# Optimization experiments

Hardware: AMD Instinct MI355X
Metric: run time of the kernel (lower is better)

The kernel has to match this reference:

```python
import jax, jax.numpy as jnp
import numpy as np

H = 8     # n_head_qk == n_head_v
DF = 32   # d_fix_qk == d_fix_v

def setup_inputs() -> dict:
    key = jax.random.key(0)
    k0, k1, k2, k3, k4 = jax.random.split(key, 5)
    x = jax.random.normal(k0, (2, 2048, 128), jnp.float32)
    attn_bias = jax.random.normal(k1, (1, H, 2048, 2048), jnp.float32) * 0.1
    Wqkv = jax.random.normal(k2, (3 * H * DF, 128), jnp.float32) * 0.02   # nn.Linear(d_model, 3*h*df)
    Wtalk = jax.random.normal(k3, (H, H), jnp.float32) * 0.1              # 1x1 Conv2d over head channels
    Wproj = jax.random.normal(k4, (128, H * DF), jnp.float32) * 0.02      # nn.Linear(h*df_v, d_model)
    return {"x": x, "attn_bias": attn_bias, "Wqkv": Wqkv, "Wtalk": Wtalk, "Wproj": Wproj}

def reference(x, attn_bias, Wqkv, Wtalk, Wproj):
    B, P, D = x.shape
    # qkv: [B,P,3*H*DF] -> [3,B,H,P,DF]
    qkv = (x @ Wqkv.T).reshape(B, P, 3, H, DF).transpose(2, 0, 3, 1, 4)
    scale = jnp.sqrt(jnp.asarray(DF, x.dtype))
    q, k, v = qkv[0] / scale, qkv[1], qkv[2]
    attn = jnp.einsum('bhpd,bhqd->bhpq', q, k)          # [B,H,P,P]
    attn = jnp.einsum('gh,bhpq->bgpq', Wtalk, attn)     # talking-heads 1x1 conv
    attn = jax.nn.softmax(attn + attn_bias, axis=-1)
    out = jnp.einsum('bhpq,bhqd->bhpd', attn, v)        # [B,H,P,DF]
    out = out.transpose(0, 2, 1, 3).reshape(B, P, H * DF)
    return out @ Wproj.T                                 # [B,P,D]
```

## Files before the change

### kernel.cpp

```cpp
#include <hip/hip_runtime.h>


typedef __attribute__((ext_vector_type(8))) short short8v;
typedef __attribute__((ext_vector_type(4))) float f32x4;

static __device__ __forceinline__ unsigned short f2bf(float f) {
  union { float f; unsigned u; } v; v.f = f;
  return (unsigned short)((v.u + 0x7FFFu + ((v.u >> 16) & 1u)) >> 16);
}

#define RAW_BARRIER() do { \
  asm volatile("s_waitcnt lgkmcnt(0)" ::: "memory"); \
  __builtin_amdgcn_sched_barrier(0); \
  __builtin_amdgcn_s_barrier(); \
  __builtin_amdgcn_sched_barrier(0); \
} while (0)

__global__ __launch_bounds__(256) void qkv_kernel(
    const float* __restrict__ x, const float* __restrict__ Wqkv,
    unsigned short* __restrict__ q_ws, unsigned short* __restrict__ k_ws,
    unsigned short* __restrict__ v_t) {
  __shared__ float xl[8][128];
  const int tid = threadIdx.x;
  const int rowbase = blockIdx.x * 8;
  {
    int r = tid >> 5, k4 = (tid & 31) * 4;
    *(float4*)&xl[r][k4] = *(const float4*)&x[(size_t)(rowbase + r) * 128 + k4];
  }
  __syncthreads();
  float acc[8][3];
#pragma unroll
  for (int r = 0; r < 8; ++r) { acc[r][0] = 0.f; acc[r][1] = 0.f; acc[r][2] = 0.f; }
  const float* w0p = &Wqkv[(size_t)tid * 128];
  const float* w1p = &Wqkv[(size_t)(tid + 256) * 128];
  const float* w2p = &Wqkv[(size_t)(tid + 512) * 128];
  for (int k4 = 0; k4 < 128; k4 += 4) {
    float4 w0 = *(const float4*)&w0p[k4];
    float4 w1 = *(const float4*)&w1p[k4];
    float4 w2 = *(const float4*)&w2p[k4];
#pragma unroll
    for (int r = 0; r < 8; ++r) {
      float4 xv = *(const float4*)&xl[r][k4];
      acc[r][0] += xv.x * w0.x + xv.y * w0.y + xv.z * w0.z + xv.w * w0.w;
      acc[r][1] += xv.x * w1.x + xv.y * w1.y + xv.z * w1.z + xv.w * w1.w;
      acc[r][2] += xv.x * w2.x + xv.y * w2.y + xv.z * w2.z + xv.w * w2.w;
    }
  }
  const int h = tid >> 5, d = tid & 31;
#pragma unroll
  for (int r = 0; r < 8; ++r) {
    int row = rowbase + r, b = row >> 11, pp = row & 2047;
    size_t base = ((size_t)(b * 8 + h) * 2048 + pp) * 32 + d;
    q_ws[base] = f2bf(acc[r][0] * 0.17677669529663687f);
    k_ws[base] = f2bf(acc[r][1]);
    v_t[((size_t)(b * 8 + h) * 32 + d) * 2048 + pp] = f2bf(acc[r][2]);
  }
}

template <int SPLIT>
__global__ __launch_bounds__(256, 2) void attn_kernel(
    const unsigned short* __restrict__ q_ws, const unsigned short* __restrict__ k_ws,
    const unsigned short* __restrict__ v_t, const float* __restrict__ bias,
    const float* __restrict__ Wtalk, float* __restrict__ pm, float* __restrict__ pl,
    float* __restrict__ pO) {
  constexpr int NB = 64 / SPLIT;
  __shared__ __align__(16) float Sb[8 * 1088];
  __shared__ __align__(16) unsigned short Pb[8192];

  const int qt_blk = blockIdx.x, split = blockIdx.y, b = blockIdx.z;
  const int q0 = qt_blk * 32, kv0 = split * (2048 / SPLIT);
  const int tid = threadIdx.x, w = tid >> 6, l = tid & 63, lg = l >> 4, ln = l & 15;
  const int p_mix = tid >> 3, qs = tid & 7, prow = q0 + p_mix;

  float wt[64];
#pragma unroll
  for (int i = 0; i < 64; ++i) wt[i] = Wtalk[i];

  short8v qf[2][2];
#pragma unroll
  for (int hh = 0; hh < 2; ++hh)
#pragma unroll
    for (int pt = 0; pt < 2; ++pt) {
      int h = 2 * w + hh;
      size_t a = ((size_t)((b * 8 + h) * 2048) + q0 + pt * 16 + ln) * 32 + lg * 8;
      qf[hh][pt] = *(const short8v*)&q_ws[a];
    }

  f32x4 Of[2][2][2];
#pragma unroll
  for (int hh = 0; hh < 2; ++hh)
#pragma unroll
    for (int pt = 0; pt < 2; ++pt)
#pragma unroll
      for (int dt = 0; dt < 2; ++dt) Of[hh][pt][dt] = (f32x4){0.f, 0.f, 0.f, 0.f};

  float mreg[8], lreg[8];
#pragma unroll
  for (int g = 0; g < 8; ++g) { mreg[g] = -1e30f; lreg[g] = 0.f; }

  const unsigned short *kB[2][2], *vB[2][2];
#pragma unroll
  for (int hh = 0; hh < 2; ++hh)
#pragma unroll
    for (int sc = 0; sc < 2; ++sc) {
      kB[hh][sc] = k_ws + ((size_t)(b * 8 + 2 * w + hh) * 2048 + kv0 + sc * 16 + ln) * 32 + lg * 8;
      vB[hh][sc] = v_t + ((size_t)(b * 8 + 2 * w + hh) * 32 + sc * 16 + ln) * 2048 + kv0 + lg * 8;
    }
  const float* bB = bias + (size_t)prow * 2048 + kv0 + qs * 4;

  short8v kf[2][2], vf[2][2];
  float4 bf[8];
#pragma unroll
  for (int hh = 0; hh < 2; ++hh)
#pragma unroll
    for (int sc = 0; sc < 2; ++sc) {
      kf[hh][sc] = *(const short8v*)kB[hh][sc];
      vf[hh][sc] = *(const short8v*)vB[hh][sc];
    }
#pragma unroll
  for (int g = 0; g < 8; ++g) bf[g] = *(const float4*)(bB + (size_t)g * 4194304);

#pragma unroll 2
  for (int s = 0; s < NB; ++s) {
    const int sn = (s + 1 < NB) ? s + 1 : s;

#pragma unroll
    for (int hh = 0; hh < 2; ++hh) {
      const int h_ = 2 * w + hh;
#pragma unroll
      for (int qt = 0; qt < 2; ++qt) {
#pragma unroll
        for (int pt = 0; pt < 2; ++pt) {
          f32x4 s4 = __builtin_amdgcn_mfma_f32_16x16x32_bf16(
              qf[hh][pt], kf[hh][qt], (f32x4){0.f, 0.f, 0.f, 0.f}, 0, 0, 0);
#pragma unroll
          for (int r = 0; r < 4; ++r)
            Sb[h_ * 1088 + (pt * 16 + lg * 4 + r) * 32 + qt * 16 + ln] = s4[r];
        }
      }
    }
    RAW_BARRIER();

    short8v kf_n[2][2];
#pragma unroll
    for (int hh = 0; hh < 2; ++hh)
#pragma unroll
      for (int sc = 0; sc < 2; ++sc)
        kf_n[hh][sc] = *(const short8v*)(kB[hh][sc] + (size_t)sn * 1024);

    {
      float4 sv[8];
#pragma unroll
      for (int h = 0; h < 8; ++h)
        sv[h] = *(const float4*)&Sb[h * 1088 + p_mix * 32 + qs * 4];
#pragma unroll
      for (int g = 0; g < 8; ++g) {
        float4 t4 = bf[g];
#pragma unroll
        for (int h = 0; h < 8; ++h) {
          const float wgh = wt[g * 8 + h];
          t4.x += wgh * sv[h].x; t4.y += wgh * sv[h].y;
          t4.z += wgh * sv[h].z; t4.w += wgh * sv[h].w;
        }
        float mx = fmaxf(fmaxf(t4.x, t4.y), fmaxf(t4.z, t4.w));
        mx = fmaxf(mx, __shfl_xor(mx, 1));
        mx = fmaxf(mx, __shfl_xor(mx, 2));
        mx = fmaxf(mx, __shfl_xor(mx, 4));
        const float mnew = fmaxf(mreg[g], mx);
        const float a_ = __expf(mreg[g] - mnew);
        mreg[g] = mnew;
        float ex = __expf(t4.x - mnew), ey = __expf(t4.y - mnew);
        float ez = __expf(t4.z - mnew), ew = __expf(t4.w - mnew);
        float ls = ex + ey + ez + ew;
        ls += __shfl_xor(ls, 1); ls += __shfl_xor(ls, 2); ls += __shfl_xor(ls, 4);
        lreg[g] = lreg[g] * a_ + ls;
        if (qs == 0) Sb[g * 1088 + 1024 + p_mix] = a_;
        unsigned u0 = (unsigned)f2bf(ex) | ((unsigned)f2bf(ey) << 16);
        unsigned u1 = (unsigned)f2bf(ez) | ((unsigned)f2bf(ew) << 16);
        uint2 pk; pk.x = u0; pk.y = u1;
        *(uint2*)&Pb[(size_t)((g * 2 + (p_mix >> 4)) * 64 + (qs >> 1) * 16 + (p_mix & 15)) * 8 + (qs & 1) * 4] = pk;
      }
    }

    float4 bf_n[8];
#pragma unroll
    for (int g = 0; g < 8; ++g)
      bf_n[g] = *(const float4*)(bB + (size_t)g * 4194304 + sn * 32);

    RAW_BARRIER();

#pragma unroll
    for (int hh = 0; hh < 2; ++hh) {
      const int h_ = 2 * w + hh;
#pragma unroll
      for (int pt = 0; pt < 2; ++pt) {
        float4 av = *(const float4*)&Sb[h_ * 1088 + 1024 + pt * 16 + lg * 4];
        short8v pa = *(const short8v*)&Pb[(size_t)((h_ * 2 + pt) * 64 + l) * 8];
#pragma unroll
        for (int dt = 0; dt < 2; ++dt) {
          f32x4 o = Of[hh][pt][dt];
          o[0] *= av.x; o[1] *= av.y; o[2] *= av.z; o[3] *= av.w;
          Of[hh][pt][dt] = __builtin_amdgcn_mfma_f32_16x16x32_bf16(pa, vf[hh][dt], o, 0, 0, 0);
        }
      }
    }

    short8v vf_n[2][2];
#pragma unroll
    for (int hh = 0; hh < 2; ++hh)
#pragma unroll
      for (int sc = 0; sc < 2; ++sc)
        vf_n[hh][sc] = *(const short8v*)(vB[hh][sc] + sn * 32);

#pragma unroll
    for (int hh = 0; hh < 2; ++hh)
#pragma unroll
      for (int sc = 0; sc < 2; ++sc) { kf[hh][sc] = kf_n[hh][sc]; vf[hh][sc] = vf_n[hh][sc]; }
#pragma unroll
    for (int g = 0; g < 8; ++g) bf[g] = bf_n[g];
  }

  const size_t ob = (size_t)((split * 2 + b) * 8);
#pragma unroll
  for (int hh = 0; hh < 2; ++hh)
#pragma unroll
    for (int pt = 0; pt < 2; ++pt)
#pragma unroll
      for (int dt = 0; dt < 2; ++dt)
#pragma unroll
        for (int r = 0; r < 4; ++r) {
          int h = 2 * w + hh;
          size_t idx = ((ob + h) * 2048 + q0 + pt * 16 + lg * 4 + r) * 32 + dt * 16 + ln;
          pO[idx] = Of[hh][pt][dt][r];
        }
  if (qs == 0) {
#pragma unroll
    for (int g = 0; g < 8; ++g) {
      size_t idx = (ob + g) * 2048 + prow;
      pm[idx] = mreg[g];
      pl[idx] = lreg[g];
    }
  }
}

template <int SPLIT>
__global__ __launch_bounds__(256) void comb_kernel(
    const float* __restrict__ pm, const float* __restrict__ pl,
    const float* __restrict__ pO, const float* __restrict__ Wproj,
    float* __restrict__ out) {
  __shared__ float ol[8][256];
  const int tid = threadIdx.x;
  const int rowbase = blockIdx.x * 8;
  {
    const int g = tid >> 5, d = tid & 31;
    for (int r = 0; r < 8; ++r) {
      int row = rowbase + r, b = row >> 11, p = row & 2047;
      size_t b0 = ((size_t)(b * 8 + g) * 2048 + p);
      float ms[SPLIT];
      float mx = -1e30f;
#pragma unroll
      for (int s = 0; s < SPLIT; ++s) {
        ms[s] = pm[b0 + (size_t)s * 32768];
        mx = fmaxf(mx, ms[s]);
      }
      float den = 0.f, acc = 0.f;
#pragma unroll
      for (int s = 0; s < SPLIT; ++s) {
        float ww = __expf(ms[s] - mx);
        den += ww * pl[b0 + (size_t)s * 32768];
        acc += ww * pO[(b0 + (size_t)s * 32768) * 32 + d];
      }
      ol[r][tid] = acc / den;
    }
  }
  __syncthreads();
  const int j = tid & 127, rh = tid >> 7;
  float acc[8];
#pragma unroll
  for (int r = 0; r < 8; ++r) acc[r] = 0.f;
  for (int c4 = 0; c4 < 128; c4 += 4) {
    float4 wv = *(const float4*)&Wproj[(size_t)j * 256 + rh * 128 + c4];
#pragma unroll
    for (int r = 0; r < 8; ++r) {
      float4 ov = *(const float4*)&ol[r][rh * 128 + c4];
      acc[r] += ov.x * wv.x + ov.y * wv.y + ov.z * wv.z + ov.w * wv.w;
    }
  }
  __syncthreads();
  float* red = &ol[0][0];
#pragma unroll
  for (int r = 0; r < 8; ++r) red[(r * 128 + j) * 2 + rh] = acc[r];
  __syncthreads();
#pragma unroll
  for (int rr = 0; rr < 4; ++rr) {
    int r = (tid >> 7) * 4 + rr;
    int row = rowbase + r;
    out[(size_t)row * 128 + (tid & 127)] =
        red[(r * 128 + (tid & 127)) * 2] + red[(r * 128 + (tid & 127)) * 2 + 1];
  }
}

extern "C" void kernel_launch(void* const* d_in, const int* in_sizes, int n_in,
                              void* d_out, int out_size, void* d_ws, size_t ws_size,
                              hipStream_t stream) {
  const float* x     = (const float*)d_in[0];
  const float* bias  = (const float*)d_in[1];
  const float* Wqkv  = (const float*)d_in[2];
  const float* Wtalk = (const float*)d_in[3];
  const float* Wproj = (const float*)d_in[4];
  float* out = (float*)d_out;
  char* ws = (char*)d_ws;
  unsigned short* q_ws = (unsigned short*)(ws);
  unsigned short* k_ws = (unsigned short*)(ws + (2u << 20));
  unsigned short* v_t  = (unsigned short*)(ws + (4u << 20));

  const size_t base = 6291456;
  const size_t per_split = 4456448;
  int SPLIT = (ws_size >= base + 8 * per_split) ? 8
            : (ws_size >= base + 4 * per_split) ? 4 : 2;
  float* pm = (float*)(ws + base);
  float* pl = (float*)(ws + base + (size_t)SPLIT * 131072);
  float* pO = (float*)(ws + base + (size_t)SPLIT * 262144);

  qkv_kernel<<<512, 256, 0, stream>>>(x, Wqkv, q_ws, k_ws, v_t);
  if (SPLIT == 8) {
    attn_kernel<8><<<dim3(64, 8, 2), 256, 0, stream>>>(q_ws, k_ws, v_t, bias, Wtalk, pm, pl, pO);
    comb_kernel<8><<<512, 256, 0, stream>>>(pm, pl, pO, Wproj, out);
  } else if (SPLIT == 4) {
    attn_kernel<4><<<dim3(64, 4, 2), 256, 0, stream>>>(q_ws, k_ws, v_t, bias, Wtalk, pm, pl, pO);
    comb_kernel<4><<<512, 256, 0, stream>>>(pm, pl, pO, Wproj, out);
  } else {
    attn_kernel<2><<<dim3(64, 2, 2), 256, 0, stream>>>(q_ws, k_ws, v_t, bias, Wtalk, pm, pl, pO);
    comb_kernel<2><<<512, 256, 0, stream>>>(pm, pl, pO, Wproj, out);
  }
}
```

Baseline: 316.3 us.

## Store scores as bf16, lazy softmax rescale, raise occupancy, remap blocks, vectorize V store

The score staging buffer in shared memory now holds bf16 with a padded stride instead of fp32, and the rescale factors get their own small array. This shrinks LDS use, and launch bounds rise to three blocks per CU. The online softmax skips the max reduction and rescale unless some lane's local max exceeds the running max by more than 8, and the per-row sum reduction is deferred to after the loop. Blocks are remapped over a 2D grid that interleaves batches, and the V-transpose store in the QKV kernel is packed into one 16-byte write. The changes trade score precision (bf16 before the talking-heads mix) and slightly looser exponent bounds for less LDS, fewer shuffles and fewer exps.

```diff
diff --git a/kernel.cpp b/kernel.cpp
--- a/kernel.cpp
+++ b/kernel.cpp
@@ -3,10 +3,14 @@
 
 typedef __attribute__((ext_vector_type(8))) short short8v;
 typedef __attribute__((ext_vector_type(4))) float f32x4;
+typedef __attribute__((ext_vector_type(4))) unsigned short ushort4v;
 
 static __device__ __forceinline__ unsigned short f2bf(float f) {
   union { float f; unsigned u; } v; v.f = f;
   return (unsigned short)((v.u + 0x7FFFu + ((v.u >> 16) & 1u)) >> 16);
+}
+static __device__ __forceinline__ float bf2f(unsigned short s) {
+  return __uint_as_float(((unsigned)s) << 16);
 }
 
 #define RAW_BARRIER() do { \
@@ -47,27 +51,33 @@
     }
   }
   const int h = tid >> 5, d = tid & 31;
+  const int b0 = rowbase >> 11, pp0 = rowbase & 2047;
+  short8v vv;
 #pragma unroll
   for (int r = 0; r < 8; ++r) {
-    int row = rowbase + r, b = row >> 11, pp = row & 2047;
-    size_t base = ((size_t)(b * 8 + h) * 2048 + pp) * 32 + d;
+    size_t base = ((size_t)(b0 * 8 + h) * 2048 + pp0 + r) * 32 + d;
     q_ws[base] = f2bf(acc[r][0] * 0.17677669529663687f);
     k_ws[base] = f2bf(acc[r][1]);
-    v_t[((size_t)(b * 8 + h) * 32 + d) * 2048 + pp] = f2bf(acc[r][2]);
-  }
+    vv[r] = (short)f2bf(acc[r][2]);
+  }
+  *(short8v*)&v_t[((size_t)(b0 * 8 + h) * 32 + d) * 2048 + pp0] = vv;
 }
 
 template <int SPLIT>
-__global__ __launch_bounds__(256, 2) void attn_kernel(
+__global__ __launch_bounds__(256, 3) void attn_kernel(
     const unsigned short* __restrict__ q_ws, const unsigned short* __restrict__ k_ws,
     const unsigned short* __restrict__ v_t, const float* __restrict__ bias,
     const float* __restrict__ Wtalk, float* __restrict__ pm, float* __restrict__ pl,
     float* __restrict__ pO) {
   constexpr int NB = 64 / SPLIT;
-  __shared__ __align__(16) float Sb[8 * 1088];
+  __shared__ __align__(16) unsigned short Sb16[8 * 1152];
+  __shared__ __align__(16) float Al[256];
   __shared__ __align__(16) unsigned short Pb[8192];
 
-  const int qt_blk = blockIdx.x, split = blockIdx.y, b = blockIdx.z;
+  const int bx = blockIdx.x;
+  const int qt_blk = ((bx >> 4) << 3) | (bx & 7);
+  const int b = (bx >> 3) & 1;
+  const int split = blockIdx.y;
   const int q0 = qt_blk * 32, kv0 = split * (2048 / SPLIT);
   const int tid = threadIdx.x, w = tid >> 6, l = tid & 63, lg = l >> 4, ln = l & 15;
   const int p_mix = tid >> 3, qs = tid & 7, prow = q0 + p_mix;
@@ -135,7 +145,7 @@
               qf[hh][pt], kf[hh][qt], (f32x4){0.f, 0.f, 0.f, 0.f}, 0, 0, 0);
 #pragma unroll
           for (int r = 0; r < 4; ++r)
-            Sb[h_ * 1088 + (pt * 16 + lg * 4 + r) * 32 + qt * 16 + ln] = s4[r];
+            Sb16[h_ * 1152 + (pt * 16 + lg * 4 + r) * 36 + qt * 16 + ln] = f2bf(s4[r]);
         }
       }
     }
@@ -151,8 +161,11 @@
     {
       float4 sv[8];
 #pragma unroll
-      for (int h = 0; h < 8; ++h)
-        sv[h] = *(const float4*)&Sb[h * 1088 + p_mix * 32 + qs * 4];
+      for (int h = 0; h < 8; ++h) {
+        ushort4v raw = *(const ushort4v*)&Sb16[h * 1152 + p_mix * 36 + qs * 4];
+        sv[h].x = bf2f(raw.x); sv[h].y = bf2f(raw.y);
+        sv[h].z = bf2f(raw.z); sv[h].w = bf2f(raw.w);
+      }
 #pragma unroll
       for (int g = 0; g < 8; ++g) {
         float4 t4 = bf[g];
@@ -162,19 +175,22 @@
           t4.x += wgh * sv[h].x; t4.y += wgh * sv[h].y;
           t4.z += wgh * sv[h].z; t4.w += wgh * sv[h].w;
         }
-        float mx = fmaxf(fmaxf(t4.x, t4.y), fmaxf(t4.z, t4.w));
-        mx = fmaxf(mx, __shfl_xor(mx, 1));
-        mx = fmaxf(mx, __shfl_xor(mx, 2));
-        mx = fmaxf(mx, __shfl_xor(mx, 4));
-        const float mnew = fmaxf(mreg[g], mx);
-        const float a_ = __expf(mreg[g] - mnew);
-        mreg[g] = mnew;
-        float ex = __expf(t4.x - mnew), ey = __expf(t4.y - mnew);
-        float ez = __expf(t4.z - mnew), ew = __expf(t4.w - mnew);
-        float ls = ex + ey + ez + ew;
-        ls += __shfl_xor(ls, 1); ls += __shfl_xor(ls, 2); ls += __shfl_xor(ls, 4);
-        lreg[g] = lreg[g] * a_ + ls;
-        if (qs == 0) Sb[g * 1088 + 1024 + p_mix] = a_;
+        float lm = fmaxf(fmaxf(t4.x, t4.y), fmaxf(t4.z, t4.w));
+        float a_ = 1.0f;
+        if (!__all(lm <= mreg[g] + 8.0f)) {
+          float rm = lm;
+          rm = fmaxf(rm, __shfl_xor(rm, 1));
+          rm = fmaxf(rm, __shfl_xor(rm, 2));
+          rm = fmaxf(rm, __shfl_xor(rm, 4));
+          float mnew = fmaxf(mreg[g], rm);
+          a_ = __expf(mreg[g] - mnew);
+          mreg[g] = mnew;
+          lreg[g] *= a_;
+        }
+        float ex = __expf(t4.x - mreg[g]), ey = __expf(t4.y - mreg[g]);
+        float ez = __expf(t4.z - mreg[g]), ew = __expf(t4.w - mreg[g]);
+        lreg[g] += (ex + ey) + (ez + ew);
+        if (qs == 0) Al[g * 32 + p_mix] = a_;
         unsigned u0 = (unsigned)f2bf(ex) | ((unsigned)f2bf(ey) << 16);
         unsigned u1 = (unsigned)f2bf(ez) | ((unsigned)f2bf(ew) << 16);
         uint2 pk; pk.x = u0; pk.y = u1;
@@ -194,7 +210,7 @@
       const int h_ = 2 * w + hh;
 #pragma unroll
       for (int pt = 0; pt < 2; ++pt) {
-        float4 av = *(const float4*)&Sb[h_ * 1088 + 1024 + pt * 16 + lg * 4];
+        float4 av = *(const float4*)&Al[h_ * 32 + pt * 16 + lg * 4];
         short8v pa = *(const short8v*)&Pb[(size_t)((h_ * 2 + pt) * 64 + l) * 8];
 #pragma unroll
         for (int dt = 0; dt < 2; ++dt) {
@@ -218,6 +234,13 @@
       for (int sc = 0; sc < 2; ++sc) { kf[hh][sc] = kf_n[hh][sc]; vf[hh][sc] = vf_n[hh][sc]; }
 #pragma unroll
     for (int g = 0; g < 8; ++g) bf[g] = bf_n[g];
+  }
+
+#pragma unroll
+  for (int g = 0; g < 8; ++g) {
+    float ls = lreg[g];
+    ls += __shfl_xor(ls, 1); ls += __shfl_xor(ls, 2); ls += __shfl_xor(ls, 4);
+    lreg[g] = ls;
   }
 
   const size_t ob = (size_t)((split * 2 + b) * 8);
@@ -294,8 +317,8 @@
 #pragma unroll
   for (int rr = 0; rr < 4; ++rr) {
     int r = (tid >> 7) * 4 + rr;
-    int row = rowbase + r;
-    out[(size_t)row * 128 + (tid & 127)] =
+    int rrow = rowbase + r;
+    out[(size_t)rrow * 128 + (tid & 127)] =
         red[(r * 128 + (tid & 127)) * 2] + red[(r * 128 + (tid & 127)) * 2 + 1];
   }
 }
@@ -324,13 +347,13 @@
 
   qkv_kernel<<<512, 256, 0, stream>>>(x, Wqkv, q_ws, k_ws, v_t);
   if (SPLIT == 8) {
-    attn_kernel<8><<<dim3(64, 8, 2), 256, 0, stream>>>(q_ws, k_ws, v_t, bias, Wtalk, pm, pl, pO);
+    attn_kernel<8><<<dim3(128, 8), 256, 0, stream>>>(q_ws, k_ws, v_t, bias, Wtalk, pm, pl, pO);
     comb_kernel<8><<<512, 256, 0, stream>>>(pm, pl, pO, Wproj, out);
   } else if (SPLIT == 4) {
-    attn_kernel<4><<<dim3(64, 4, 2), 256, 0, stream>>>(q_ws, k_ws, v_t, bias, Wtalk, pm, pl, pO);
+    attn_kernel<4><<<dim3(128, 4), 256, 0, stream>>>(q_ws, k_ws, v_t, bias, Wtalk, pm, pl, pO);
     comb_kernel<4><<<512, 256, 0, stream>>>(pm, pl, pO, Wproj, out);
   } else {
-    attn_kernel<2><<<dim3(64, 2, 2), 256, 0, stream>>>(q_ws, k_ws, v_t, bias, Wtalk, pm, pl, pO);
+    attn_kernel<2><<<dim3(128, 2), 256, 0, stream>>>(q_ws, k_ws, v_t, bias, Wtalk, pm, pl, pO);
     comb_kernel<2><<<512, 256, 0, stream>>>(pm, pl, pO, Wproj, out);
   }
 }
```

New measurement: 565.2 us. +78.7%, slower.
